# Optimization experiments

Measured on AMD Instinct MI355X. Metric: run time of the kernel, lower is better.

The kernel has to match this reference:

```python
import jax, jax.numpy as jnp
import numpy as np

B, S, H = 2, 2048, 2048
NH, NKV, HD = 16, 4, 128
THETA = 1000000.0

def _rope_tables(seq_len, dim, theta):
    inv_freq = 1.0 / (theta ** (np.arange(0, dim, 2, dtype=np.float32) / dim))
    t = np.arange(seq_len, dtype=np.float32)
    freqs = np.outer(t, inv_freq)                      # [S, dim/2]
    emb = np.concatenate([freqs, freqs], axis=-1)      # [S, dim]
    return jnp.asarray(np.cos(emb)), jnp.asarray(np.sin(emb))

def setup_inputs() -> dict:
    key = jax.random.key(0)
    ks = jax.random.split(key, 5)
    cos, sin = _rope_tables(S, HD, THETA)
    scale = 1.0 / np.sqrt(H)
    return {
        "x": jax.random.normal(ks[0], (B, S, H), jnp.float32),
        "cos": cos, "sin": sin,
        "wq": jax.random.normal(ks[1], (H, NH * HD), jnp.float32) * scale,
        "wk": jax.random.normal(ks[2], (H, NKV * HD), jnp.float32) * scale,
        "wv": jax.random.normal(ks[3], (H, NKV * HD), jnp.float32) * scale,
        "wo": jax.random.normal(ks[4], (NH * HD, H), jnp.float32) * scale,
    }

def _rotate_half(t):
    h = t.shape[-1] // 2
    return jnp.concatenate([-t[..., h:], t[..., :h]], axis=-1)

def reference(x, cos, sin, wq, wk, wv, wo):
    b, s, _ = x.shape
    n_rep = NH // NKV
    q = (x @ wq).reshape(b, s, NH, HD)    # [b,s,nh,hd]
    k = (x @ wk).reshape(b, s, NKV, HD)
    v = (x @ wv).reshape(b, s, NKV, HD)
    # RoPE: cos/sin [s,hd] broadcast over batch and heads
    c = cos[None, :, None, :]
    sn = sin[None, :, None, :]
    q = q * c + _rotate_half(q) * sn
    k = k * c + _rotate_half(k) * sn
    # GQA: repeat kv heads n_rep times
    k = jnp.repeat(k, n_rep, axis=2)      # [b,s,nh,hd]
    v = jnp.repeat(v, n_rep, axis=2)
    q = q.transpose(0, 2, 1, 3)           # [b,nh,s,hd]
    k = k.transpose(0, 2, 1, 3)
    v = v.transpose(0, 2, 1, 3)
    scores = jnp.einsum('bhqd,bhkd->bhqk', q, k) / jnp.sqrt(jnp.float32(HD))
    causal = jnp.tril(jnp.ones((s, s), dtype=bool))
    scores = jnp.where(causal[None, None], scores, jnp.float32(-jnp.inf))
    attn = jax.nn.softmax(scores.astype(jnp.float32), axis=-1).astype(q.dtype)
    out = jnp.einsum('bhqk,bhkd->bhqd', attn, v)
    out = out.transpose(0, 2, 1, 3).reshape(b, s, NH * HD)
    return out @ wo
```

## Files before the change

kernel.cpp:

```cpp
#include <hip/hip_runtime.h>
#include <hip/hip_bf16.h>

#define Bb 2
#define Ss 2048
#define Hh 2048
#define NH 16
#define NKV 4
#define HD 128
#define NREP (NH / NKV)
#define Mrows (Bb * Ss)
#define NQKV (NH*HD + 2*NKV*HD)

using short8 = __attribute__((ext_vector_type(8))) short;
using f32x4  = __attribute__((ext_vector_type(4))) float;

__device__ __forceinline__ unsigned short f2b(float f) {
  union { float f; unsigned u; } v; v.f = f;
  return (unsigned short)((v.u + 0x7fffu + ((v.u >> 16) & 1u)) >> 16);
}

__device__ __forceinline__ void gload16(const void* g, void* l) {
  __builtin_amdgcn_global_load_lds(
      (const __attribute__((address_space(1))) unsigned int*)g,
      (__attribute__((address_space(3))) unsigned int*)l, 16, 0, 0);
}

__global__ void prep(const float* __restrict__ x, unsigned short* __restrict__ xb,
                     const float* __restrict__ wq, const float* __restrict__ wk,
                     const float* __restrict__ wv, unsigned short* __restrict__ wqkvt,
                     const float* __restrict__ wo, unsigned short* __restrict__ wot) {
  __shared__ float tile[32][33];
  const int bid = blockIdx.x;
  const int t = threadIdx.x;
  if (bid < 8192) {
    int i = (bid * 256 + t) * 4;
    float4 f = *(const float4*)(x + i);
    ushort4 o;
    o.x = f2b(f.x); o.y = f2b(f.y); o.z = f2b(f.z); o.w = f2b(f.w);
    *(ushort4*)(xb + i) = o;
    return;
  }
  const int tx = t & 31, ty = t >> 5;
  if (bid < 8192 + 6144) {
    int idx = bid - 8192;
    int n0 = (idx % 96) * 32, k0 = (idx / 96) * 32;
    const float* src; int c0, C;
    if (n0 < Hh)            { src = wq; c0 = n0;            C = NH * HD; }
    else if (n0 < Hh + 512) { src = wk; c0 = n0 - Hh;       C = NKV * HD; }
    else                    { src = wv; c0 = n0 - Hh - 512; C = NKV * HD; }
    #pragma unroll
    for (int i = ty; i < 32; i += 8)
      tile[i][tx] = src[(long)(k0 + i) * C + c0 + tx];
    __syncthreads();
    #pragma unroll
    for (int i = ty; i < 32; i += 8)
      wqkvt[(long)(n0 + i) * Hh + k0 + tx] = f2b(tile[tx][i]);
  } else {
    int idx = bid - 8192 - 6144;
    int n0 = (idx % 64) * 32, k0 = (idx / 64) * 32;
    #pragma unroll
    for (int i = ty; i < 32; i += 8)
      tile[i][tx] = wo[(long)(k0 + i) * Hh + n0 + tx];
    __syncthreads();
    #pragma unroll
    for (int i = ty; i < 32; i += 8)
      wot[(long)(n0 + i) * Hh + k0 + tx] = f2b(tile[tx][i]);
  }
}

__global__ __launch_bounds__(128) void gemm_qkv(const unsigned short* __restrict__ A,
                                                const unsigned short* __restrict__ Bt,
                                                const float* __restrict__ cosT,
                                                const float* __restrict__ sinT,
                                                unsigned short* __restrict__ qt,
                                                unsigned short* __restrict__ kt,
                                                unsigned short* __restrict__ vt) {
  __shared__ unsigned short As[128 * 64];
  __shared__ unsigned short Bs[128 * 64];
  const int t = threadIdx.x;
  const int lane = t & 63, wave = t >> 6;
  const int quad = lane >> 4, l16 = lane & 15;
  const int tile = blockIdx.x >> 5;
  const int n0 = tile * 128, m0 = (blockIdx.x & 31) * 128;
  const int wm = wave * 64;
  const bool isv = tile >= 20;
  const int Kk = Hh;

  f32x4 acc[4][8] = {};

  const int srow8 = t >> 3;
  const int sgr   = (t & 7) ^ (srow8 & 7);
  const unsigned short* Ag = A  + (long)(m0 + srow8) * Kk + sgr * 8;
  const unsigned short* Bg = Bt + (long)(n0 + srow8) * Kk + sgr * 8;
  unsigned short* lA = As + (wave * 64) * 8;
  unsigned short* lB = Bs + (wave * 64) * 8;

  for (int k0 = 0; k0 < Kk; k0 += 64) {
    #pragma unroll
    for (int i = 0; i < 8; i++)
      gload16(Ag + (long)(i * 16) * Kk + k0, lA + i * 128 * 8);
    #pragma unroll
    for (int i = 0; i < 8; i++)
      gload16(Bg + (long)(i * 16) * Kk + k0, lB + i * 128 * 8);
    __syncthreads();

    #pragma unroll
    for (int sub = 0; sub < 2; sub++) {
      const int slot = ((sub * 4 + quad) ^ (l16 & 7)) * 8;
      short8 af[4], bf[8];
      #pragma unroll
      for (int i = 0; i < 4; i++)
        af[i] = *(const short8*)(As + (wm + i * 16 + l16) * 64 + slot);
      #pragma unroll
      for (int i = 0; i < 8; i++)
        bf[i] = *(const short8*)(Bs + (i * 16 + l16) * 64 + slot);

      if (isv) {
        #pragma unroll
        for (int mi = 0; mi < 4; mi++)
          #pragma unroll
          for (int ni = 0; ni < 8; ni++)
            acc[mi][ni] = __builtin_amdgcn_mfma_f32_16x16x32_bf16(bf[ni], af[mi], acc[mi][ni], 0, 0, 0);
      } else {
        #pragma unroll
        for (int mi = 0; mi < 4; mi++)
          #pragma unroll
          for (int ni = 0; ni < 8; ni++)
            acc[mi][ni] = __builtin_amdgcn_mfma_f32_16x16x32_bf16(af[mi], bf[ni], acc[mi][ni], 0, 0, 0);
      }
    }
    __syncthreads();
  }

  if (!isv) {
    const bool isq = tile < 16;
    const int hh = isq ? tile : tile - 16;
    #pragma unroll
    for (int mi = 0; mi < 4; mi++)
      #pragma unroll
      for (int r = 0; r < 4; r++) {
        int srw = m0 + wm + mi * 16 + quad * 4 + r;
        int bb = srw >> 11, s = srw & (Ss - 1);
        unsigned short* dst = isq ? qt + (((long)bb * NH + hh) * Ss + s) * HD
                                  : kt + (((long)bb * NKV + hh) * Ss + s) * HD;
        const float* cr = cosT + (long)s * HD;
        const float* sr = sinT + (long)s * HD;
        #pragma unroll
        for (int ni = 0; ni < 4; ni++) {
          int d = ni * 16 + l16;
          float cc = cr[d], sn = sr[d];
          float x0 = acc[mi][ni][r], x1 = acc[mi][ni + 4][r];
          dst[d]      = f2b(x0 * cc - x1 * sn);
          dst[d + 64] = f2b(x1 * cc + x0 * sn);
        }
      }
  } else {
    const int kvh = tile - 20;
    const int bb = m0 >> 11;
    #pragma unroll
    for (int mi = 0; mi < 4; mi++)
      #pragma unroll
      for (int ni = 0; ni < 8; ni++)
        #pragma unroll
        for (int r = 0; r < 4; r++) {
          int d = ni * 16 + quad * 4 + r;
          int s = (m0 + wm + mi * 16 + l16) & (Ss - 1);
          vt[(((long)bb * NKV + kvh) * HD + d) * Ss + s] = f2b(acc[mi][ni][r]);
        }
  }
}

__global__ __launch_bounds__(256) void gemm_bt(const unsigned short* __restrict__ A,
                                               const unsigned short* __restrict__ Bt,
                                               float* __restrict__ Cv,
                                               int Mm, int Nn, int Kk) {
  __shared__ unsigned short As[128 * 64];
  __shared__ unsigned short Bs[128 * 64];
  const int t = threadIdx.x;
  const int lane = t & 63, wave = t >> 6;
  const int quad = lane >> 4, l16 = lane & 15;
  const int n0 = (blockIdx.x >> 5) * 128, m0 = (blockIdx.x & 31) * 128;
  const int wm = (wave >> 1) * 64, wn = (wave & 1) * 64;

  f32x4 acc[4][4] = {};

  const int srow = t >> 3;
  const int sgr  = (t & 7) ^ (srow & 7);
  const unsigned short* Ag = A  + (long)(m0 + srow) * Kk + sgr * 8;
  const unsigned short* Bg = Bt + (long)(n0 + srow) * Kk + sgr * 8;
  unsigned short* lA = As + (wave * 64) * 8;
  unsigned short* lB = Bs + (wave * 64) * 8;

  for (int k0 = 0; k0 < Kk; k0 += 64) {
    #pragma unroll
    for (int i = 0; i < 4; i++)
      gload16(Ag + (long)i * 32 * Kk + k0, lA + i * 256 * 8);
    #pragma unroll
    for (int i = 0; i < 4; i++)
      gload16(Bg + (long)i * 32 * Kk + k0, lB + i * 256 * 8);
    __syncthreads();

    #pragma unroll
    for (int sub = 0; sub < 2; sub++) {
      short8 af[4], bf[4];
      #pragma unroll
      for (int i = 0; i < 4; i++)
        af[i] = *(const short8*)(As + (wm + i * 16 + l16) * 64 + (((sub * 4 + quad) ^ (l16 & 7)) * 8));
      #pragma unroll
      for (int i = 0; i < 4; i++)
        bf[i] = *(const short8*)(Bs + (wn + i * 16 + l16) * 64 + (((sub * 4 + quad) ^ (l16 & 7)) * 8));

      #pragma unroll
      for (int mi = 0; mi < 4; mi++)
        #pragma unroll
        for (int ni = 0; ni < 4; ni++)
          acc[mi][ni] = __builtin_amdgcn_mfma_f32_16x16x32_bf16(af[mi], bf[ni], acc[mi][ni], 0, 0, 0);
    }
    __syncthreads();
  }

  #pragma unroll
  for (int mi = 0; mi < 4; mi++)
    #pragma unroll
    for (int ni = 0; ni < 4; ni++)
      #pragma unroll
      for (int r = 0; r < 4; r++) {
        long row = m0 + wm + mi * 16 + quad * 4 + r;
        long col = n0 + wn + ni * 16 + l16;
        Cv[row * Nn + col] = acc[mi][ni][r];
      }
}

__global__ __launch_bounds__(256, 2) void flash_attn(const unsigned short* __restrict__ qt,
                                                     const unsigned short* __restrict__ kt,
                                                     const unsigned short* __restrict__ vt,
                                                     unsigned short* __restrict__ out) {
  __shared__ unsigned short Ks[2][64 * 128];
  __shared__ unsigned short Vs[2][128 * 64];

  const int w = threadIdx.x >> 6, lane = threadIdx.x & 63;
  const int quad = lane >> 4, l16 = lane & 15;
  const int r8 = lane >> 3, c8 = lane & 7;
  const int idx = blockIdx.x;
  const int xcd = idx & 7;
  const int b = xcd >> 2, kvh = xcd & 3;
  const int rest = idx >> 3;
  const int k16 = rest >> 2;
  const int qblk = (k16 < 8) ? (15 - k16) : (k16 - 8);
  const int h = kvh * NREP + (rest & 3);
  const int q0w = qblk * 128 + w * 32;

  const unsigned short* Qb = qt + ((long)b * NH + h) * Ss * HD;
  const unsigned short* Kb = kt + ((long)b * NKV + kvh) * Ss * HD;
  const unsigned short* Vb = vt + ((long)b * NKV + kvh) * HD * Ss;
  const int nch = (qblk + 1) * 2;

  #pragma unroll
  for (int i = 0; i < 4; i++) {
    int rho = i * 16 + w * 4 + quad;
    int key = (rho & 32) + ((rho >> 2) & 3) * 8 + ((rho >> 4) & 1) * 4 + (rho & 3);
    int sg = l16 ^ (w * 4 + quad);
    gload16(Kb + (long)key * HD + sg * 8, &Ks[0][(i * 256 + w * 64) * 8]);
  }
  #pragma unroll
  for (int i = 0; i < 4; i++) {
    int dv = i * 32 + w * 8 + r8;
    int sg = c8 ^ r8;
    gload16(Vb + (long)dv * Ss + sg * 8, &Vs[0][(i * 256 + w * 64) * 8]);
  }

  short8 qf[2][4];
  #pragma unroll
  for (int qi = 0; qi < 2; qi++)
    #pragma unroll
    for (int kc = 0; kc < 4; kc++)
      qf[qi][kc] = *(const short8*)(Qb + (long)(q0w + qi * 16 + l16) * HD + kc * 32 + quad * 8);

  f32x4 accO[2][8] = {};
  float l_i[2];
  l_i[0] = l_i[1] = 0.f;
  const float cscale = 1.4426950408889634f * 0.08838834764831845f;

  for (int c = 0; c < nch; ++c) {
    const unsigned short* Ksb = Ks[c & 1];
    const unsigned short* Vsb = Vs[c & 1];

    if (c + 1 < nch) {
      const int k0 = (c + 1) * 64;
      unsigned short* Kd = Ks[(c + 1) & 1];
      unsigned short* Vd = Vs[(c + 1) & 1];
      #pragma unroll
      for (int i = 0; i < 4; i++) {
        int rho = i * 16 + w * 4 + quad;
        int key = (rho & 32) + ((rho >> 2) & 3) * 8 + ((rho >> 4) & 1) * 4 + (rho & 3);
        int sg = l16 ^ (w * 4 + quad);
        gload16(Kb + (long)(k0 + key) * HD + sg * 8, Kd + (i * 256 + w * 64) * 8);
      }
      #pragma unroll
      for (int i = 0; i < 4; i++) {
        int dv = i * 32 + w * 8 + r8;
        int sg = c8 ^ r8;
        gload16(Vb + (long)dv * Ss + k0 + sg * 8, Vd + (i * 256 + w * 64) * 8);
      }
      asm volatile("s_waitcnt vmcnt(8)" ::: "memory");
    } else {
      asm volatile("s_waitcnt vmcnt(0)" ::: "memory");
    }
    asm volatile("s_barrier" ::: "memory");

    if (c * 64 < q0w + 32) {
      f32x4 sc[2][4] = {};
      #pragma unroll
      for (int T = 0; T < 4; T++)
        #pragma unroll
        for (int kc = 0; kc < 4; kc++) {
          short8 kf = *(const short8*)(Ksb + ((16 * T + l16) * 16 + ((kc * 4 + quad) ^ l16)) * 8);
          #pragma unroll
          for (int qi = 0; qi < 2; qi++)
            sc[qi][T] = __builtin_amdgcn_mfma_f32_16x16x32_bf16(kf, qf[qi][kc], sc[qi][T], 0, 0, 0);
        }

      if ((c + 1) * 64 - 1 > q0w) {
        #pragma unroll
        for (int qi = 0; qi < 2; qi++) {
          int qq = q0w + qi * 16 + l16;
          #pragma unroll
          for (int T = 0; T < 4; T++)
            #pragma unroll
            for (int r = 0; r < 4; r++) {
              int ka = c * 64 + (T >> 1) * 32 + quad * 8 + (T & 1) * 4 + r;
              if (ka > qq) sc[qi][T][r] = -__builtin_inff();
            }
        }
      }

      short8 pf[2][2];
      #pragma unroll
      for (int qi = 0; qi < 2; qi++) {
        float p[4][4], rs = 0.f;
        #pragma unroll
        for (int T = 0; T < 4; T++)
          #pragma unroll
          for (int r = 0; r < 4; r++) {
            p[T][r] = __builtin_amdgcn_exp2f(sc[qi][T][r] * cscale);
            rs += p[T][r];
          }
        rs += __shfl_xor(rs, 16);
        rs += __shfl_xor(rs, 32);
        l_i[qi] += rs;

        #pragma unroll
        for (int c2 = 0; c2 < 2; c2++) {
          short8 f;
          f[0] = (short)f2b(p[2 * c2][0]);     f[1] = (short)f2b(p[2 * c2][1]);
          f[2] = (short)f2b(p[2 * c2][2]);     f[3] = (short)f2b(p[2 * c2][3]);
          f[4] = (short)f2b(p[2 * c2 + 1][0]); f[5] = (short)f2b(p[2 * c2 + 1][1]);
          f[6] = (short)f2b(p[2 * c2 + 1][2]); f[7] = (short)f2b(p[2 * c2 + 1][3]);
          pf[qi][c2] = f;
        }
      }

      #pragma unroll
      for (int c2 = 0; c2 < 2; c2++)
        #pragma unroll
        for (int Dt = 0; Dt < 8; Dt++) {
          short8 vf = *(const short8*)(Vsb + ((16 * Dt + l16) * 8 + ((4 * c2 + quad) ^ (l16 & 7))) * 8);
          #pragma unroll
          for (int qi = 0; qi < 2; qi++)
            accO[qi][Dt] = __builtin_amdgcn_mfma_f32_16x16x32_bf16(vf, pf[qi][c2], accO[qi][Dt], 0, 0, 0);
        }
    }

    asm volatile("s_waitcnt lgkmcnt(0)" ::: "memory");
    asm volatile("s_barrier" ::: "memory");
  }

  #pragma unroll
  for (int qi = 0; qi < 2; qi++) {
    float inv = 1.f / l_i[qi];
    long orow = (long)b * Ss + q0w + qi * 16 + l16;
    #pragma unroll
    for (int Dt = 0; Dt < 8; Dt++) {
      ushort4 o;
      o.x = f2b(accO[qi][Dt][0] * inv);
      o.y = f2b(accO[qi][Dt][1] * inv);
      o.z = f2b(accO[qi][Dt][2] * inv);
      o.w = f2b(accO[qi][Dt][3] * inv);
      *(ushort4*)(out + orow * (NH * HD) + h * HD + Dt * 16 + quad * 4) = o;
    }
  }
}

extern "C" void kernel_launch(void* const* d_in, const int* in_sizes, int n_in,
                              void* d_out, int out_size, void* d_ws, size_t ws_size,
                              hipStream_t stream) {
  const float* x    = (const float*)d_in[0];
  const float* cosT = (const float*)d_in[1];
  const float* sinT = (const float*)d_in[2];
  const float* wq   = (const float*)d_in[3];
  const float* wk   = (const float*)d_in[4];
  const float* wv   = (const float*)d_in[5];
  const float* wo   = (const float*)d_in[6];
  float* out = (float*)d_out;

  char* ws = (char*)d_ws;
  unsigned short* xb    = (unsigned short*)(ws);
  unsigned short* wqkvt = (unsigned short*)(ws + (16l << 20));
  unsigned short* wot   = (unsigned short*)(ws + (28l << 20));
  unsigned short* qt    = (unsigned short*)(ws + (36l << 20));
  unsigned short* kt    = (unsigned short*)(ws + (52l << 20));
  unsigned short* vt    = (unsigned short*)(ws + (56l << 20));
  unsigned short* attno = xb;

  prep<<<8192 + 6144 + 4096, 256, 0, stream>>>(x, xb, wq, wk, wv, wqkvt, wo, wot);

  gemm_qkv<<<(NQKV / 128) * (Mrows / 128), 128, 0, stream>>>(xb, wqkvt, cosT, sinT, qt, kt, vt);

  flash_attn<<<(Ss / 128) * NH * Bb, 256, 0, stream>>>(qt, kt, vt, attno);

  gemm_bt<<<(Hh / 128) * (Mrows / 128), 256, 0, stream>>>(attno, wot, out, Mrows, Hh, Hh);
}
```

Before: 326.4 us.

## Split QKV GEMM across four waves with permuted weight columns for local RoPE

The QKV projection GEMM moves from 2 waves (each 64x128) to 4 waves in a 2x2 layout, each owning a 64x64 sub-tile, which halves accumulator registers per thread and doubles threads per block. To keep the RoPE pairing (d, d+64) inside a single wave's columns, the prep kernel now permutes the Q and K weight columns within each head. Paired halves then sit in adjacent 16-column fragments. The epilogue index math is updated to match. This trades extra prep indexing and smaller per-wave reuse for higher occupancy and more waves for latency hiding.

```diff
diff --git a/kernel.cpp b/kernel.cpp
--- a/kernel.cpp
+++ b/kernel.cpp
@@ -44,13 +44,20 @@
   if (bid < 8192 + 6144) {
     int idx = bid - 8192;
     int n0 = (idx % 96) * 32, k0 = (idx / 96) * 32;
-    const float* src; int c0, C;
-    if (n0 < Hh)            { src = wq; c0 = n0;            C = NH * HD; }
-    else if (n0 < Hh + 512) { src = wk; c0 = n0 - Hh;       C = NKV * HD; }
-    else                    { src = wv; c0 = n0 - Hh - 512; C = NKV * HD; }
+    const float* src; int base, C;
+    if (n0 < Hh)            { src = wq; base = 0;        C = NH * HD; }
+    else if (n0 < Hh + 512) { src = wk; base = Hh;       C = NKV * HD; }
+    else                    { src = wv; base = Hh + 512; C = NKV * HD; }
+    int ng = n0 + tx;
+    int cmg = ng;
+    if (ng < Hh + 512) {
+      int j = ng & 127;
+      cmg = (ng & ~127) + ((j >> 5) << 4) + (j & 15) + ((j >> 4) & 1) * 64;
+    }
+    int col = cmg - base;
     #pragma unroll
     for (int i = ty; i < 32; i += 8)
-      tile[i][tx] = src[(long)(k0 + i) * C + c0 + tx];
+      tile[i][tx] = src[(long)(k0 + i) * C + col];
     __syncthreads();
     #pragma unroll
     for (int i = ty; i < 32; i += 8)
@@ -68,7 +75,7 @@
   }
 }
 
-__global__ __launch_bounds__(128) void gemm_qkv(const unsigned short* __restrict__ A,
+__global__ __launch_bounds__(256) void gemm_qkv(const unsigned short* __restrict__ A,
                                                 const unsigned short* __restrict__ Bt,
                                                 const float* __restrict__ cosT,
                                                 const float* __restrict__ sinT,
@@ -82,50 +89,50 @@
   const int quad = lane >> 4, l16 = lane & 15;
   const int tile = blockIdx.x >> 5;
   const int n0 = tile * 128, m0 = (blockIdx.x & 31) * 128;
-  const int wm = wave * 64;
+  const int wm = (wave >> 1) * 64, wn = (wave & 1) * 64;
   const bool isv = tile >= 20;
   const int Kk = Hh;
 
-  f32x4 acc[4][8] = {};
-
-  const int srow8 = t >> 3;
-  const int sgr   = (t & 7) ^ (srow8 & 7);
-  const unsigned short* Ag = A  + (long)(m0 + srow8) * Kk + sgr * 8;
-  const unsigned short* Bg = Bt + (long)(n0 + srow8) * Kk + sgr * 8;
+  f32x4 acc[4][4] = {};
+
+  const int srow = t >> 3;
+  const int sgr  = (t & 7) ^ (srow & 7);
+  const unsigned short* Ag = A  + (long)(m0 + srow) * Kk + sgr * 8;
+  const unsigned short* Bg = Bt + (long)(n0 + srow) * Kk + sgr * 8;
   unsigned short* lA = As + (wave * 64) * 8;
   unsigned short* lB = Bs + (wave * 64) * 8;
 
   for (int k0 = 0; k0 < Kk; k0 += 64) {
     #pragma unroll
-    for (int i = 0; i < 8; i++)
-      gload16(Ag + (long)(i * 16) * Kk + k0, lA + i * 128 * 8);
-    #pragma unroll
-    for (int i = 0; i < 8; i++)
-      gload16(Bg + (long)(i * 16) * Kk + k0, lB + i * 128 * 8);
+    for (int i = 0; i < 4; i++)
+      gload16(Ag + (long)i * 32 * Kk + k0, lA + i * 256 * 8);
+    #pragma unroll
+    for (int i = 0; i < 4; i++)
+      gload16(Bg + (long)i * 32 * Kk + k0, lB + i * 256 * 8);
     __syncthreads();
 
     #pragma unroll
     for (int sub = 0; sub < 2; sub++) {
       const int slot = ((sub * 4 + quad) ^ (l16 & 7)) * 8;
-      short8 af[4], bf[8];
+      short8 af[4], bf[4];
       #pragma unroll
       for (int i = 0; i < 4; i++)
         af[i] = *(const short8*)(As + (wm + i * 16 + l16) * 64 + slot);
       #pragma unroll
-      for (int i = 0; i < 8; i++)
-        bf[i] = *(const short8*)(Bs + (i * 16 + l16) * 64 + slot);
+      for (int i = 0; i < 4; i++)
+        bf[i] = *(const short8*)(Bs + (wn + i * 16 + l16) * 64 + slot);
 
       if (isv) {
         #pragma unroll
         for (int mi = 0; mi < 4; mi++)
           #pragma unroll
-          for (int ni = 0; ni < 8; ni++)
+          for (int ni = 0; ni < 4; ni++)
             acc[mi][ni] = __builtin_amdgcn_mfma_f32_16x16x32_bf16(bf[ni], af[mi], acc[mi][ni], 0, 0, 0);
       } else {
         #pragma unroll
         for (int mi = 0; mi < 4; mi++)
           #pragma unroll
-          for (int ni = 0; ni < 8; ni++)
+          for (int ni = 0; ni < 4; ni++)
             acc[mi][ni] = __builtin_amdgcn_mfma_f32_16x16x32_bf16(af[mi], bf[ni], acc[mi][ni], 0, 0, 0);
       }
     }
@@ -146,10 +153,10 @@
         const float* cr = cosT + (long)s * HD;
         const float* sr = sinT + (long)s * HD;
         #pragma unroll
-        for (int ni = 0; ni < 4; ni++) {
-          int d = ni * 16 + l16;
+        for (int ni = 0; ni < 4; ni += 2) {
+          int d = (((wn + ni * 16) >> 5) << 4) + l16;
           float cc = cr[d], sn = sr[d];
-          float x0 = acc[mi][ni][r], x1 = acc[mi][ni + 4][r];
+          float x0 = acc[mi][ni][r], x1 = acc[mi][ni + 1][r];
           dst[d]      = f2b(x0 * cc - x1 * sn);
           dst[d + 64] = f2b(x1 * cc + x0 * sn);
         }
@@ -160,10 +167,10 @@
     #pragma unroll
     for (int mi = 0; mi < 4; mi++)
       #pragma unroll
-      for (int ni = 0; ni < 8; ni++)
+      for (int ni = 0; ni < 4; ni++)
         #pragma unroll
         for (int r = 0; r < 4; r++) {
-          int d = ni * 16 + quad * 4 + r;
+          int d = wn + ni * 16 + quad * 4 + r;
           int s = (m0 + wm + mi * 16 + l16) & (Ss - 1);
           vt[(((long)bb * NKV + kvh) * HD + d) * Ss + s] = f2b(acc[mi][ni][r]);
         }
@@ -414,7 +421,7 @@
 
   prep<<<8192 + 6144 + 4096, 256, 0, stream>>>(x, xb, wq, wk, wv, wqkvt, wo, wot);
 
-  gemm_qkv<<<(NQKV / 128) * (Mrows / 128), 128, 0, stream>>>(xb, wqkvt, cosT, sinT, qt, kt, vt);
+  gemm_qkv<<<(NQKV / 128) * (Mrows / 128), 256, 0, stream>>>(xb, wqkvt, cosT, sinT, qt, kt, vt);
 
   flash_attn<<<(Ss / 128) * NH * Bb, 256, 0, stream>>>(qt, kt, vt, attno);
 
```

Result: faster. 310.8 us (-4.8%).
